# Kernel tuning notes

Measured on AMD Instinct MI355X. Metric: run time of the kernel, lower is better.

Reference implementation:

```python
import jax, jax.numpy as jnp
import numpy as np

B, T, H = 65536, 24, 64  # batch, input_window_size, num_neurons
SLOPE = 25.0             # snntorch fast_sigmoid default slope

@jax.custom_vjp
def spike(x):
    # heaviside forward, fast-sigmoid surrogate backward
    return (x > 0).astype(x.dtype)

def _spike_fwd(x):
    return (x > 0).astype(x.dtype), x

def _spike_bwd(x, g):
    return (g / (SLOPE * jnp.abs(x) + 1.0) ** 2,)

spike.defvjp(_spike_fwd, _spike_bwd)

def slstm_cell(x, syn, mem, Wih, Whh, bih, bhh, thr):
    # snntorch SLSTM: LSTMCell with h=mem, c=syn; reset_mechanism='subtract'
    reset = jax.lax.stop_gradient((mem - thr > 0).astype(x.dtype))
    gates = x @ Wih.T + bih + mem @ Whh.T + bhh  # (B, 4H)
    i, f, g, o = jnp.split(gates, 4, axis=-1)
    syn_new = jax.nn.sigmoid(f) * syn + jax.nn.sigmoid(i) * jnp.tanh(g)
    mem_new = jax.nn.sigmoid(o) * jnp.tanh(syn_new) - reset * thr
    spk = spike(mem_new - thr)
    return spk, syn_new, mem_new

def setup_inputs() -> dict:
    key = jax.random.key(0)
    ks = jax.random.split(key, 11)
    s = float(1.0 / np.sqrt(H))  # LSTMCell uniform init bound
    so = float(1.0 / np.sqrt((T + 2) * H))
    u = lambda k, shape: jax.random.uniform(k, shape, jnp.float32, -s, s)
    return {
        "x": jax.random.normal(ks[0], (B, T, 1), jnp.float32),
        "Wih1": u(ks[1], (4 * H, 1)),
        "Whh1": u(ks[2], (4 * H, H)),
        "bih1": u(ks[3], (4 * H,)),
        "bhh1": u(ks[4], (4 * H,)),
        "thr1": jnp.float32(0.5),
        "Wih2": u(ks[5], (4 * H, H)),
        "Whh2": u(ks[6], (4 * H, H)),
        "bih2": u(ks[7], (4 * H,)),
        "bhh2": u(ks[8], (4 * H,)),
        "thr2": jnp.float32(0.5),
        "Wout": jax.random.uniform(ks[9], (2, (T + 2) * H), jnp.float32, -so, so),
        "bout": jnp.array([0.2, -0.2], jnp.float32),
    }

def reference(x, Wih1, Whh1, bih1, bhh1, thr1,
              Wih2, Whh2, bih2, bhh2, thr2, Wout, bout):
    Bn = x.shape[0]
    Hn = Whh1.shape[1]
    z = jnp.zeros((Bn, Hn), x.dtype)
    carry0 = (z, z, z, z)  # syn1, mem1, syn2, mem2

    def step(carry, xt):
        syn1, mem1, syn2, mem2 = carry
        spk1, syn1, mem1 = slstm_cell(xt, syn1, mem1, Wih1, Whh1, bih1, bhh1, thr1)
        spk2, syn2, mem2 = slstm_cell(spk1, syn2, mem2, Wih2, Whh2, bih2, bhh2, thr2)
        return (syn1, mem1, syn2, mem2), spk2

    (syn1, mem1, syn2, mem2), spk2_seq = jax.lax.scan(
        step, carry0, jnp.swapaxes(x, 0, 1))  # spk2_seq: (T, B, H)
    # extra step: feed mem1 into slstm2
    spk2_last, syn2, mem2 = slstm_cell(mem1, syn2, mem2, Wih2, Whh2, bih2, bhh2, thr2)
    lst = jnp.concatenate(
        [jnp.swapaxes(spk2_seq, 0, 1).reshape(Bn, -1), spk2_last, mem2], axis=1)
    return lst @ Wout.T + bout  # (B, 2)
```

## Files before the change

kernel.cpp:

```cpp
#include <hip/hip_runtime.h>
#include <cstdint>
#include <cstddef>


#define BB 65536
#define TT 24
#define NB 8

__device__ __forceinline__ float bcastf(float v, int l) {
  return __int_as_float(__builtin_amdgcn_readlane(__float_as_int(v), l));
}
__device__ __forceinline__ float sigm(float v) {
  return __fdividef(1.0f, 1.0f + __expf(-v));
}
__device__ __forceinline__ float tanh_fast(float v) {
  return fmaf(-2.0f, __fdividef(1.0f, __expf(2.0f * v) + 1.0f), 1.0f);
}
__device__ __forceinline__ float wsum(float v) {
#pragma unroll
  for (int o = 32; o > 0; o >>= 1) v += __shfl_xor(v, o);
  return v;
}

__global__ __attribute__((amdgpu_waves_per_eu(4, 4))) __launch_bounds__(512)
void snn_pass1(
    const float* __restrict__ x, const float* __restrict__ Wih1,
    const float* __restrict__ Whh1, const float* __restrict__ bih1,
    const float* __restrict__ bhh1, const float* __restrict__ thr1p,
    unsigned long long* __restrict__ spk_out, float* __restrict__ mem1_out) {
  __shared__ float4 P1[64][64];
  __shared__ float stM[8][64][NB];
  int tid = threadIdx.x;
  int lane = tid & 63, wave = tid >> 6;
  int wb = (blockIdx.x * 8 + wave) * NB;

  float xv[NB];
  int lt = (lane < TT) ? lane : (TT - 1);
#pragma unroll
  for (int b = 0; b < NB; b++) xv[b] = x[(size_t)(wb + b) * TT + lt];

  for (int idx = tid; idx < 16384; idx += 512) {
    int k = idx >> 6, m = idx & 63;
    ((float*)&P1[m][k & 63])[k >> 6] = Whh1[idx];
  }
  __syncthreads();
  float thr1 = thr1p[0];
  float b1q[4], wq[4];
#pragma unroll
  for (int q = 0; q < 4; q++) {
    b1q[q] = bih1[q * 64 + lane] + bhh1[q * 64 + lane];
    wq[q] = Wih1[q * 64 + lane];
  }
  float syn[NB], mem[NB];
#pragma unroll
  for (int b = 0; b < NB; b++) { syn[b] = 0.0f; mem[b] = 0.0f; }

  for (int t = 0; t < TT; t++) {
#pragma unroll
    for (int b = 0; b < NB; b++) stM[wave][lane][b] = mem[b];
    unsigned long long myspk = 0;
#pragma unroll
    for (int h = 0; h < 2; h++) {
      const int B0 = h * 4;
      float acc[4][4];
#pragma unroll
      for (int j = 0; j < 4; j++) {
        float xbt = bcastf(xv[B0 + j], t);
#pragma unroll
        for (int q = 0; q < 4; q++) acc[j][q] = fmaf(xbt, wq[q], b1q[q]);
      }
#pragma unroll 8
      for (int m = 0; m < 64; m++) {
        float4 w = P1[m][lane];
        float4 sa = *(const float4*)&stM[wave][m][B0];
        float s[4] = {sa.x, sa.y, sa.z, sa.w};
#pragma unroll
        for (int j = 0; j < 4; j++) {
          acc[j][0] = fmaf(s[j], w.x, acc[j][0]);
          acc[j][1] = fmaf(s[j], w.y, acc[j][1]);
          acc[j][2] = fmaf(s[j], w.z, acc[j][2]);
          acc[j][3] = fmaf(s[j], w.w, acc[j][3]);
        }
      }
#pragma unroll
      for (int j = 0; j < 4; j++) {
        int b = B0 + j;
        float ig = sigm(acc[j][0]), fg = sigm(acc[j][1]);
        float gg = tanh_fast(acc[j][2]), og = sigm(acc[j][3]);
        float sn = fmaf(fg, syn[b], ig * gg);
        float rst = (mem[b] > thr1) ? thr1 : 0.0f;
        float mn = fmaf(og, tanh_fast(sn), -rst);
        syn[b] = sn;
        mem[b] = mn;
        unsigned long long msk = __ballot(mn > thr1);
        if (lane == b) myspk = msk;
      }
      __builtin_amdgcn_sched_barrier(0);
    }
    if (lane < NB)
      spk_out[(size_t)t * BB + wb + lane] = myspk;
  }
#pragma unroll
  for (int b = 0; b < NB; b++)
    mem1_out[(size_t)(wb + b) * 64 + lane] = mem[b];
}

__global__ __attribute__((amdgpu_waves_per_eu(4, 4))) __launch_bounds__(1024)
void snn_pass2(
    const float* __restrict__ Wih2, const float* __restrict__ Whh2,
    const float* __restrict__ bih2, const float* __restrict__ bhh2,
    const float* __restrict__ thr2p, const float* __restrict__ Wout,
    const float* __restrict__ bout,
    const unsigned long long* __restrict__ spk_in,
    const float* __restrict__ mem1_in, float* __restrict__ out) {
  __shared__ float4 Pih[64][64];
  __shared__ float4 Phh[64][64];
  __shared__ float stM[16][64][NB];
  int tid = threadIdx.x;
  int lane = tid & 63, wave = tid >> 6;
  int wb = (blockIdx.x * 16 + wave) * NB;

  unsigned long long raw[NB];
#pragma unroll
  for (int b = 0; b < NB; b++) raw[b] = spk_in[(size_t)0 * BB + wb + b];

  for (int idx = tid; idx < 16384; idx += 1024) {
    int k = idx >> 6, m = idx & 63;
    ((float*)&Pih[m][k & 63])[k >> 6] = Wih2[idx];
    ((float*)&Phh[m][k & 63])[k >> 6] = Whh2[idx];
  }
  __syncthreads();
  float thr2 = thr2p[0];
  float b2q[4];
#pragma unroll
  for (int q = 0; q < 4; q++) b2q[q] = bih2[q * 64 + lane] + bhh2[q * 64 + lane];
  float syn[NB], mem[NB];
  unsigned sb8[NB];
#pragma unroll
  for (int b = 0; b < NB; b++) { syn[b] = 0.0f; mem[b] = 0.0f; sb8[b] = 0u; }

  for (int t = 0; t < TT; t++) {
    unsigned long long mk[NB];
#pragma unroll
    for (int b = 0; b < NB; b++) {
      unsigned lo = __builtin_amdgcn_readfirstlane((unsigned)raw[b]);
      unsigned hi = __builtin_amdgcn_readfirstlane((unsigned)(raw[b] >> 32));
      mk[b] = ((unsigned long long)hi << 32) | (unsigned long long)lo;
    }
    if (t + 1 < TT) {
#pragma unroll
      for (int b = 0; b < NB; b++)
        raw[b] = spk_in[(size_t)(t + 1) * BB + wb + b];
    }
#pragma unroll
    for (int b = 0; b < NB; b++) stM[wave][lane][b] = mem[b];
#pragma unroll
    for (int h = 0; h < 2; h++) {
      const int B0 = h * 4;
      float acc[4][4];
#pragma unroll
      for (int j = 0; j < 4; j++) {
#pragma unroll
        for (int q = 0; q < 4; q++) acc[j][q] = b2q[q];
      }
#pragma unroll 4
      for (int m = 0; m < 64; m++) {
        float4 wh = Phh[m][lane];
        float4 sa = *(const float4*)&stM[wave][m][B0];
        float s[4] = {sa.x, sa.y, sa.z, sa.w};
#pragma unroll
        for (int j = 0; j < 4; j++) {
          acc[j][0] = fmaf(s[j], wh.x, acc[j][0]);
          acc[j][1] = fmaf(s[j], wh.y, acc[j][1]);
          acc[j][2] = fmaf(s[j], wh.z, acc[j][2]);
          acc[j][3] = fmaf(s[j], wh.w, acc[j][3]);
        }
      }
#pragma unroll
      for (int j = 0; j < 4; j++) {
        int b = B0 + j;
        unsigned long long k = mk[b];
        while (__builtin_popcountll(k) >= 4) {
          int m0 = __builtin_ctzll(k); k &= k - 1;
          int m1 = __builtin_ctzll(k); k &= k - 1;
          int m2 = __builtin_ctzll(k); k &= k - 1;
          int m3 = __builtin_ctzll(k); k &= k - 1;
          float4 r0 = Pih[m0][lane];
          float4 r1 = Pih[m1][lane];
          float4 r2 = Pih[m2][lane];
          float4 r3 = Pih[m3][lane];
          acc[j][0] += r0.x; acc[j][1] += r0.y; acc[j][2] += r0.z; acc[j][3] += r0.w;
          acc[j][0] += r1.x; acc[j][1] += r1.y; acc[j][2] += r1.z; acc[j][3] += r1.w;
          acc[j][0] += r2.x; acc[j][1] += r2.y; acc[j][2] += r2.z; acc[j][3] += r2.w;
          acc[j][0] += r3.x; acc[j][1] += r3.y; acc[j][2] += r3.z; acc[j][3] += r3.w;
        }
        while (k) {
          int m0 = __builtin_ctzll(k); k &= k - 1;
          float4 r0 = Pih[m0][lane];
          acc[j][0] += r0.x; acc[j][1] += r0.y; acc[j][2] += r0.z; acc[j][3] += r0.w;
        }
        float ig = sigm(acc[j][0]), fg = sigm(acc[j][1]);
        float gg = tanh_fast(acc[j][2]), og = sigm(acc[j][3]);
        float sn = fmaf(fg, syn[b], ig * gg);
        float rst = (mem[b] > thr2) ? thr2 : 0.0f;
        float mn = fmaf(og, tanh_fast(sn), -rst);
        syn[b] = sn;
        mem[b] = mn;
        sb8[b] |= (mn > thr2) ? (1u << t) : 0u;
      }
      __builtin_amdgcn_sched_barrier(0);
    }
  }

  float m1[NB];
#pragma unroll
  for (int b = 0; b < NB; b++) m1[b] = mem1_in[(size_t)(wb + b) * 64 + lane];
  float acc[NB][4];
#pragma unroll
  for (int b = 0; b < NB; b++) {
#pragma unroll
    for (int q = 0; q < 4; q++) acc[b][q] = b2q[q];
  }
#pragma unroll 4
  for (int m = 0; m < 64; m++) {
    float4 wi = Pih[m][lane];
    float4 wh = Phh[m][lane];
#pragma unroll
    for (int b = 0; b < NB; b++) {
      float s1 = bcastf(m1[b], m);
      float s2 = bcastf(mem[b], m);
      acc[b][0] = fmaf(s1, wi.x, fmaf(s2, wh.x, acc[b][0]));
      acc[b][1] = fmaf(s1, wi.y, fmaf(s2, wh.y, acc[b][1]));
      acc[b][2] = fmaf(s1, wi.z, fmaf(s2, wh.z, acc[b][2]));
      acc[b][3] = fmaf(s1, wi.w, fmaf(s2, wh.w, acc[b][3]));
    }
  }
  float p0[NB], p1[NB];
#pragma unroll
  for (int b = 0; b < NB; b++) { p0[b] = 0.0f; p1[b] = 0.0f; }
#pragma unroll 4
  for (int t = 0; t < TT; t++) {
    float w0 = Wout[t * 64 + lane];
    float w1 = Wout[1664 + t * 64 + lane];
#pragma unroll
    for (int b = 0; b < NB; b++) {
      float sf = ((sb8[b] >> t) & 1u) ? 1.0f : 0.0f;
      p0[b] = fmaf(sf, w0, p0[b]);
      p1[b] = fmaf(sf, w1, p1[b]);
    }
  }
  float wA0 = Wout[1536 + lane], wA1 = Wout[1664 + 1536 + lane];
  float wB0 = Wout[1600 + lane], wB1 = Wout[1664 + 1600 + lane];
  float bo0 = bout[0], bo1 = bout[1];
#pragma unroll
  for (int b = 0; b < NB; b++) {
    float ig = sigm(acc[b][0]), fg = sigm(acc[b][1]);
    float gg = tanh_fast(acc[b][2]), og = sigm(acc[b][3]);
    float sn = fmaf(fg, syn[b], ig * gg);
    float rst = (mem[b] > thr2) ? thr2 : 0.0f;
    float mn = fmaf(og, tanh_fast(sn), -rst);
    float sf = (mn > thr2) ? 1.0f : 0.0f;
    p0[b] = fmaf(sf, wA0, p0[b]);
    p1[b] = fmaf(sf, wA1, p1[b]);
    p0[b] = fmaf(mn, wB0, p0[b]);
    p1[b] = fmaf(mn, wB1, p1[b]);
  }
  float vout = 0.0f;
#pragma unroll
  for (int b = 0; b < NB; b++) {
    float r0 = wsum(p0[b]);
    float r1 = wsum(p1[b]);
    if (lane == 2 * b) vout = r0;
    if (lane == 2 * b + 1) vout = r1;
  }
  if (lane < 2 * NB)
    out[(size_t)wb * 2 + lane] = vout + ((lane & 1) ? bo1 : bo0);
}

extern "C" void kernel_launch(void* const* d_in, const int* in_sizes, int n_in,
                              void* d_out, int out_size, void* d_ws, size_t ws_size,
                              hipStream_t stream) {
  const float* x = (const float*)d_in[0];
  const float* Wih1 = (const float*)d_in[1];
  const float* Whh1 = (const float*)d_in[2];
  const float* bih1 = (const float*)d_in[3];
  const float* bhh1 = (const float*)d_in[4];
  const float* thr1 = (const float*)d_in[5];
  const float* Wih2 = (const float*)d_in[6];
  const float* Whh2 = (const float*)d_in[7];
  const float* bih2 = (const float*)d_in[8];
  const float* bhh2 = (const float*)d_in[9];
  const float* thr2 = (const float*)d_in[10];
  const float* Wout = (const float*)d_in[11];
  const float* bout = (const float*)d_in[12];

  unsigned long long* spk = (unsigned long long*)d_ws;
  float* mem1 = (float*)((char*)d_ws + (size_t)TT * BB * 8);

  snn_pass1<<<BB / (8 * NB), 512, 0, stream>>>(x, Wih1, Whh1, bih1, bhh1, thr1,
                                               spk, mem1);
  snn_pass2<<<BB / (16 * NB), 1024, 0, stream>>>(Wih2, Whh2, bih2, bhh2, thr2,
                                                 Wout, bout, spk, mem1,
                                                 (float*)d_out);
}
```

Measured before the change: 1.810 ms.

## Broadcast recurrent state via readlane and process all 8 batch rows per weight load

Removes the per-wave LDS staging buffer for the recurrent mem state. Each recurrent FMA operand is now fetched with a cross-lane readlane broadcast instead of an LDS float4 read. The two half-batch passes are merged into one 8-row loop, so each Whh weight float4 read from LDS is reused across 8 batch rows instead of 4, halving weight LDS traffic. The costs are 8 readlanes per weight row, which are serialized scalar ops, and 32 live accumulators, which raise register pressure at fixed waves_per_eu.

Measured after the change: 2.146 ms. +18.5%, slower.

```diff
diff --git a/kernel.cpp b/kernel.cpp
--- a/kernel.cpp
+++ b/kernel.cpp
@@ -29,7 +29,6 @@
     const float* __restrict__ bhh1, const float* __restrict__ thr1p,
     unsigned long long* __restrict__ spk_out, float* __restrict__ mem1_out) {
   __shared__ float4 P1[64][64];
-  __shared__ float stM[8][64][NB];
   int tid = threadIdx.x;
   int lane = tid & 63, wave = tid >> 6;
   int wb = (blockIdx.x * 8 + wave) * NB;
@@ -56,46 +55,37 @@
   for (int b = 0; b < NB; b++) { syn[b] = 0.0f; mem[b] = 0.0f; }
 
   for (int t = 0; t < TT; t++) {
-#pragma unroll
-    for (int b = 0; b < NB; b++) stM[wave][lane][b] = mem[b];
+    float acc[NB][4];
+#pragma unroll
+    for (int j = 0; j < NB; j++) {
+      float xbt = bcastf(xv[j], t);
+#pragma unroll
+      for (int q = 0; q < 4; q++) acc[j][q] = fmaf(xbt, wq[q], b1q[q]);
+    }
+#pragma unroll 8
+    for (int m = 0; m < 64; m++) {
+      float4 w = P1[m][lane];
+#pragma unroll
+      for (int j = 0; j < NB; j++) {
+        float s = bcastf(mem[j], m);
+        acc[j][0] = fmaf(s, w.x, acc[j][0]);
+        acc[j][1] = fmaf(s, w.y, acc[j][1]);
+        acc[j][2] = fmaf(s, w.z, acc[j][2]);
+        acc[j][3] = fmaf(s, w.w, acc[j][3]);
+      }
+    }
     unsigned long long myspk = 0;
 #pragma unroll
-    for (int h = 0; h < 2; h++) {
-      const int B0 = h * 4;
-      float acc[4][4];
-#pragma unroll
-      for (int j = 0; j < 4; j++) {
-        float xbt = bcastf(xv[B0 + j], t);
-#pragma unroll
-        for (int q = 0; q < 4; q++) acc[j][q] = fmaf(xbt, wq[q], b1q[q]);
-      }
-#pragma unroll 8
-      for (int m = 0; m < 64; m++) {
-        float4 w = P1[m][lane];
-        float4 sa = *(const float4*)&stM[wave][m][B0];
-        float s[4] = {sa.x, sa.y, sa.z, sa.w};
-#pragma unroll
-        for (int j = 0; j < 4; j++) {
-          acc[j][0] = fmaf(s[j], w.x, acc[j][0]);
-          acc[j][1] = fmaf(s[j], w.y, acc[j][1]);
-          acc[j][2] = fmaf(s[j], w.z, acc[j][2]);
-          acc[j][3] = fmaf(s[j], w.w, acc[j][3]);
-        }
-      }
-#pragma unroll
-      for (int j = 0; j < 4; j++) {
-        int b = B0 + j;
-        float ig = sigm(acc[j][0]), fg = sigm(acc[j][1]);
-        float gg = tanh_fast(acc[j][2]), og = sigm(acc[j][3]);
-        float sn = fmaf(fg, syn[b], ig * gg);
-        float rst = (mem[b] > thr1) ? thr1 : 0.0f;
-        float mn = fmaf(og, tanh_fast(sn), -rst);
-        syn[b] = sn;
-        mem[b] = mn;
-        unsigned long long msk = __ballot(mn > thr1);
-        if (lane == b) myspk = msk;
-      }
-      __builtin_amdgcn_sched_barrier(0);
+    for (int j = 0; j < NB; j++) {
+      float ig = sigm(acc[j][0]), fg = sigm(acc[j][1]);
+      float gg = tanh_fast(acc[j][2]), og = sigm(acc[j][3]);
+      float sn = fmaf(fg, syn[j], ig * gg);
+      float rst = (mem[j] > thr1) ? thr1 : 0.0f;
+      float mn = fmaf(og, tanh_fast(sn), -rst);
+      syn[j] = sn;
+      mem[j] = mn;
+      unsigned long long msk = __ballot(mn > thr1);
+      if (lane == j) myspk = msk;
     }
     if (lane < NB)
       spk_out[(size_t)t * BB + wb + lane] = myspk;
@@ -115,7 +105,6 @@
     const float* __restrict__ mem1_in, float* __restrict__ out) {
   __shared__ float4 Pih[64][64];
   __shared__ float4 Phh[64][64];
-  __shared__ float stM[16][64][NB];
   int tid = threadIdx.x;
   int lane = tid & 63, wave = tid >> 6;
   int wb = (blockIdx.x * 16 + wave) * NB;
@@ -152,63 +141,54 @@
       for (int b = 0; b < NB; b++)
         raw[b] = spk_in[(size_t)(t + 1) * BB + wb + b];
     }
-#pragma unroll
-    for (int b = 0; b < NB; b++) stM[wave][lane][b] = mem[b];
-#pragma unroll
-    for (int h = 0; h < 2; h++) {
-      const int B0 = h * 4;
-      float acc[4][4];
-#pragma unroll
-      for (int j = 0; j < 4; j++) {
-#pragma unroll
-        for (int q = 0; q < 4; q++) acc[j][q] = b2q[q];
-      }
-#pragma unroll 4
-      for (int m = 0; m < 64; m++) {
-        float4 wh = Phh[m][lane];
-        float4 sa = *(const float4*)&stM[wave][m][B0];
-        float s[4] = {sa.x, sa.y, sa.z, sa.w};
-#pragma unroll
-        for (int j = 0; j < 4; j++) {
-          acc[j][0] = fmaf(s[j], wh.x, acc[j][0]);
-          acc[j][1] = fmaf(s[j], wh.y, acc[j][1]);
-          acc[j][2] = fmaf(s[j], wh.z, acc[j][2]);
-          acc[j][3] = fmaf(s[j], wh.w, acc[j][3]);
-        }
-      }
-#pragma unroll
-      for (int j = 0; j < 4; j++) {
-        int b = B0 + j;
-        unsigned long long k = mk[b];
-        while (__builtin_popcountll(k) >= 4) {
-          int m0 = __builtin_ctzll(k); k &= k - 1;
-          int m1 = __builtin_ctzll(k); k &= k - 1;
-          int m2 = __builtin_ctzll(k); k &= k - 1;
-          int m3 = __builtin_ctzll(k); k &= k - 1;
-          float4 r0 = Pih[m0][lane];
-          float4 r1 = Pih[m1][lane];
-          float4 r2 = Pih[m2][lane];
-          float4 r3 = Pih[m3][lane];
-          acc[j][0] += r0.x; acc[j][1] += r0.y; acc[j][2] += r0.z; acc[j][3] += r0.w;
-          acc[j][0] += r1.x; acc[j][1] += r1.y; acc[j][2] += r1.z; acc[j][3] += r1.w;
-          acc[j][0] += r2.x; acc[j][1] += r2.y; acc[j][2] += r2.z; acc[j][3] += r2.w;
-          acc[j][0] += r3.x; acc[j][1] += r3.y; acc[j][2] += r3.z; acc[j][3] += r3.w;
-        }
-        while (k) {
-          int m0 = __builtin_ctzll(k); k &= k - 1;
-          float4 r0 = Pih[m0][lane];
-          acc[j][0] += r0.x; acc[j][1] += r0.y; acc[j][2] += r0.z; acc[j][3] += r0.w;
-        }
-        float ig = sigm(acc[j][0]), fg = sigm(acc[j][1]);
-        float gg = tanh_fast(acc[j][2]), og = sigm(acc[j][3]);
-        float sn = fmaf(fg, syn[b], ig * gg);
-        float rst = (mem[b] > thr2) ? thr2 : 0.0f;
-        float mn = fmaf(og, tanh_fast(sn), -rst);
-        syn[b] = sn;
-        mem[b] = mn;
-        sb8[b] |= (mn > thr2) ? (1u << t) : 0u;
-      }
-      __builtin_amdgcn_sched_barrier(0);
+    float acc[NB][4];
+#pragma unroll
+    for (int j = 0; j < NB; j++) {
+#pragma unroll
+      for (int q = 0; q < 4; q++) acc[j][q] = b2q[q];
+    }
+#pragma unroll 8
+    for (int m = 0; m < 64; m++) {
+      float4 wh = Phh[m][lane];
+#pragma unroll
+      for (int j = 0; j < NB; j++) {
+        float s = bcastf(mem[j], m);
+        acc[j][0] = fmaf(s, wh.x, acc[j][0]);
+        acc[j][1] = fmaf(s, wh.y, acc[j][1]);
+        acc[j][2] = fmaf(s, wh.z, acc[j][2]);
+        acc[j][3] = fmaf(s, wh.w, acc[j][3]);
+      }
+    }
+#pragma unroll
+    for (int j = 0; j < NB; j++) {
+      unsigned long long k = mk[j];
+      while (__builtin_popcountll(k) >= 4) {
+        int m0 = __builtin_ctzll(k); k &= k - 1;
+        int m1 = __builtin_ctzll(k); k &= k - 1;
+        int m2 = __builtin_ctzll(k); k &= k - 1;
+        int m3 = __builtin_ctzll(k); k &= k - 1;
+        float4 r0 = Pih[m0][lane];
+        float4 r1 = Pih[m1][lane];
+        float4 r2 = Pih[m2][lane];
+        float4 r3 = Pih[m3][lane];
+        acc[j][0] += r0.x; acc[j][1] += r0.y; acc[j][2] += r0.z; acc[j][3] += r0.w;
+        acc[j][0] += r1.x; acc[j][1] += r1.y; acc[j][2] += r1.z; acc[j][3] += r1.w;
+        acc[j][0] += r2.x; acc[j][1] += r2.y; acc[j][2] += r2.z; acc[j][3] += r2.w;
+        acc[j][0] += r3.x; acc[j][1] += r3.y; acc[j][2] += r3.z; acc[j][3] += r3.w;
+      }
+      while (k) {
+        int m0 = __builtin_ctzll(k); k &= k - 1;
+        float4 r0 = Pih[m0][lane];
+        acc[j][0] += r0.x; acc[j][1] += r0.y; acc[j][2] += r0.z; acc[j][3] += r0.w;
+      }
+      float ig = sigm(acc[j][0]), fg = sigm(acc[j][1]);
+      float gg = tanh_fast(acc[j][2]), og = sigm(acc[j][3]);
+      float sn = fmaf(fg, syn[j], ig * gg);
+      float rst = (mem[j] > thr2) ? thr2 : 0.0f;
+      float mn = fmaf(og, tanh_fast(sn), -rst);
+      syn[j] = sn;
+      mem[j] = mn;
+      sb8[j] |= (mn > thr2) ? (1u << t) : 0u;
     }
   }
 
```
